# Kernel optimization log

Hardware: AMD Instinct MI355X
Metric: run time of the kernel (lower is better)

## Reference

```python
import jax, jax.numpy as jnp
import numpy as np

E, F, H = 8, 5632, 2048
T = 8192


def setup_inputs() -> dict:
    key = jax.random.key(0)
    k1, k2, k3, k4 = jax.random.split(key, 4)
    s_w = 1.0 / np.sqrt(H)
    return {
        "expert_idx": 3,
        "hidden_states": jax.random.normal(k1, (T, H), dtype=jnp.float32),
        "fc1_1": jax.random.normal(k2, (E, F, H), dtype=jnp.float32) * s_w,
        "fc1_2": jax.random.normal(k3, (E, F, H), dtype=jnp.float32) * s_w,
        "fc2": jax.random.normal(k4, (E, H, F), dtype=jnp.float32) * (1.0 / np.sqrt(F)),
    }


def reference(expert_idx, hidden_states, fc1_1, fc1_2, fc2):
    # Select this expert's weights: [F,H], [F,H], [H,F]
    w1 = fc1_1[expert_idx]
    w2 = fc1_2[expert_idx]
    w3 = fc2[expert_idx]
    # SwiGLU FFN: silu(x @ w1^T) * (x @ w2^T) @ w3^T
    gate = jnp.einsum("th,fh->tf", hidden_states, w1)
    up = jnp.einsum("th,fh->tf", hidden_states, w2)
    fc1_out = jax.nn.silu(gate) * up  # [T, F]
    out = jnp.einsum("tf,hf->th", fc1_out, w3)  # [T, H]
    return out
```

## Files before the change

kernel.cpp:

```cpp
#include <hip/hip_runtime.h>
#include <hip/hip_bf16.h>

#define T_DIM 8192
#define H_DIM 2048
#define F_DIM 5632

typedef __attribute__((ext_vector_type(4))) float f32x4;
typedef __attribute__((ext_vector_type(8))) short bf16x8;

static __device__ __forceinline__ void gload16(const void* g, void* l) {
    __builtin_amdgcn_global_load_lds(
        (const __attribute__((address_space(1))) void*)g,
        (__attribute__((address_space(3))) void*)l,
        16, 0, 0);
}

static __device__ __forceinline__ unsigned short f2bf(float f) {
    unsigned int u = __float_as_uint(f);
    u += 0x7fffu + ((u >> 16) & 1u);
    return (unsigned short)(u >> 16);
}

__global__ __launch_bounds__(256)
void cvt_f32_bf16(const float* __restrict__ base, const int* __restrict__ eidx,
                  long per_expert, unsigned short* __restrict__ dst, long n)
{
    const float* src = base;
    if (eidx) src += (long)(*eidx) * per_expert;
    const long stride = (long)gridDim.x * blockDim.x;
    for (long i = (long)blockIdx.x * blockDim.x + threadIdx.x; i * 4 < n; i += stride) {
        const float4 v = *(const float4*)(src + i * 4);
        ushort4 o;
        o.x = f2bf(v.x); o.y = f2bf(v.y); o.z = f2bf(v.z); o.w = f2bf(v.w);
        *(ushort4*)(dst + i * 4) = o;
    }
}

static __device__ __forceinline__ void stage_half(const unsigned short* __restrict__ g,
                                                  long grow0, long ldk, long kb,
                                                  unsigned short* l, int t, int i0)
{
    const int r  = t >> 3;
    const int cc = ((t & 7) ^ (r & 7)) << 3;
    #pragma unroll
    for (int i = i0; i < i0 + 2; ++i)
        gload16(g + (grow0 + i * 64 + r) * ldk + kb + cc,
                l + i * 4096 + t * 8);
}

static __device__ __forceinline__ bf16x8 ldsfrag(const unsigned short* base,
                                                 int row, int kk, int q)
{
    return *(const bf16x8*)(base + row * 64 + (((kk * 4 + q) ^ (row & 7)) << 3));
}

#define PHASE_BODY(p, STAGE_STMT)                                              \
    {                                                                          \
        bf16x8 af[2][2];                                                       \
        _Pragma("unroll")                                                      \
        for (int l_ = 0; l_ < 2; ++l_)                                         \
            _Pragma("unroll")                                                  \
            for (int kk = 0; kk < 2; ++kk)                                     \
                af[l_][kk] = ldsfrag(la, wm * 128 + (p) * 32 + l_ * 16 + lr, kk, q); \
        STAGE_STMT;                                                            \
        __builtin_amdgcn_s_barrier();                                          \
        __builtin_amdgcn_s_setprio(1);                                         \
        _Pragma("unroll")                                                      \
        for (int l_ = 0; l_ < 2; ++l_)                                         \
            _Pragma("unroll")                                                  \
            for (int ni = 0; ni < 4; ++ni)                                     \
                _Pragma("unroll")                                              \
                for (int kk = 0; kk < 2; ++kk)                                 \
                    acc[(p) * 2 + l_][ni] = __builtin_amdgcn_mfma_f32_16x16x32_bf16( \
                        af[l_][kk], bf[ni][kk], acc[(p) * 2 + l_][ni], 0, 0, 0);     \
        __builtin_amdgcn_s_setprio(0);                                         \
        __builtin_amdgcn_s_barrier();                                          \
    }

__global__ __launch_bounds__(512, 2)
void gemm1_swiglu(const unsigned short* __restrict__ X,
                  const unsigned short* __restrict__ W1,
                  const unsigned short* __restrict__ W2,
                  unsigned short* __restrict__ Hout)
{
    __shared__ __align__(16) unsigned short sAll[4 * 16384];

    const int tid  = threadIdx.x;
    const int lane = tid & 63;
    const int wid  = tid >> 6;
    const int wm   = wid >> 2;
    const int wn   = wid & 3;
    const int q    = lane >> 4;
    const int lr   = lane & 15;

    const int nwg = gridDim.x;
    const int bid = blockIdx.x;
    const int cpx = nwg >> 3;
    const int swz = (bid & 7) * cpx + (bid >> 3);
    const int NBN = F_DIM / 128;
    const int bm  = swz / NBN;
    const int bn  = swz % NBN;

    const long arow0 = (long)bm * 256;
    const long b1r0  = (long)bn * 128;
    const long b2r0  = (long)bn * 128 - 128;
    const int  NK    = H_DIM / 64;

    f32x4 acc[8][4] = {};

    stage_half(X,  arow0, H_DIM, 0, sAll,          tid, 0);
    stage_half(X,  arow0, H_DIM, 0, sAll,          tid, 2);
    stage_half(W1, b1r0,  H_DIM, 0, sAll + 16384,  tid, 0);
    stage_half(W2, b2r0,  H_DIM, 0, sAll + 16384,  tid, 2);
    stage_half(W1, b1r0,  H_DIM, 64, sAll + 49152, tid, 0);
    stage_half(W2, b2r0,  H_DIM, 64, sAll + 49152, tid, 2);

    for (int j = 0; j < NK; ++j) {
        unsigned short* la = sAll + (j & 1) * 32768;
        unsigned short* lb = la + 16384;

        if (j + 1 < NK) {
            unsigned short* na = sAll + ((j + 1) & 1) * 32768;
            stage_half(X, arow0, H_DIM, (long)(j + 1) * 64, na, tid, 0);
            stage_half(X, arow0, H_DIM, (long)(j + 1) * 64, na, tid, 2);
            asm volatile("s_waitcnt vmcnt(8)" ::: "memory");
        } else {
            asm volatile("s_waitcnt vmcnt(0)" ::: "memory");
        }
        __builtin_amdgcn_s_barrier();

        bf16x8 bf[4][2];
        #pragma unroll
        for (int ni = 0; ni < 4; ++ni)
            #pragma unroll
            for (int kk = 0; kk < 2; ++kk)
                bf[ni][kk] = ldsfrag(lb, wn * 64 + ni * 16 + lr, kk, q);

        PHASE_BODY(0, {})
        PHASE_BODY(1, { if (j + 2 < NK) stage_half(W1, b1r0, H_DIM, (long)(j + 2) * 64, lb, tid, 0); })
        PHASE_BODY(2, { if (j + 2 < NK) stage_half(W2, b2r0, H_DIM, (long)(j + 2) * 64, lb, tid, 2); })
        PHASE_BODY(3, {})
    }

    float* slab = (float*)sAll;
    float* s = slab + (wm * 2 + (wn & 1)) * 8192;
    if (wn >= 2) {
        #pragma unroll
        for (int mi = 0; mi < 8; ++mi)
            #pragma unroll
            for (int ni = 0; ni < 4; ++ni)
                #pragma unroll
                for (int r = 0; r < 4; ++r)
                    s[(mi * 16 + q * 4 + r) * 64 + ni * 16 + lr] = acc[mi][ni][r];
    }
    __syncthreads();
    if (wn < 2) {
        const long orow = (long)bm * 256 + wm * 128;
        const long ocol = (long)bn * 128 + wn * 64;
        #pragma unroll
        for (int mi = 0; mi < 8; ++mi)
            #pragma unroll
            for (int ni = 0; ni < 4; ++ni)
                #pragma unroll
                for (int r = 0; r < 4; ++r) {
                    const float g = acc[mi][ni][r];
                    const float u = s[(mi * 16 + q * 4 + r) * 64 + ni * 16 + lr];
                    const float h = (g / (1.0f + __expf(-g))) * u;
                    Hout[(orow + mi * 16 + q * 4 + r) * F_DIM + (ocol + ni * 16 + lr)] = f2bf(h);
                }
    }
}

__global__ __launch_bounds__(512, 2)
void gemm2_out(const unsigned short* __restrict__ A,
               const unsigned short* __restrict__ B,
               float* __restrict__ Out)
{
    __shared__ __align__(16) unsigned short sAll[4 * 16384];

    const int tid  = threadIdx.x;
    const int lane = tid & 63;
    const int wid  = tid >> 6;
    const int wm   = wid >> 2;
    const int wn   = wid & 3;
    const int q    = lane >> 4;
    const int lr   = lane & 15;

    const int nwg = gridDim.x;
    const int bid = blockIdx.x;
    const int cpx = nwg >> 3;
    const int swz = (bid & 7) * cpx + (bid >> 3);
    const int NBN = H_DIM / 256;
    const int bm  = swz / NBN;
    const int bn  = swz % NBN;

    const long arow0 = (long)bm * 256;
    const long brow0 = (long)bn * 256;
    const int  NK    = F_DIM / 64;

    f32x4 acc[8][4] = {};

    stage_half(A, arow0, F_DIM, 0, sAll,          tid, 0);
    stage_half(A, arow0, F_DIM, 0, sAll,          tid, 2);
    stage_half(B, brow0, F_DIM, 0, sAll + 16384,  tid, 0);
    stage_half(B, brow0, F_DIM, 0, sAll + 16384,  tid, 2);
    stage_half(B, brow0, F_DIM, 64, sAll + 49152, tid, 0);
    stage_half(B, brow0, F_DIM, 64, sAll + 49152, tid, 2);

    for (int j = 0; j < NK; ++j) {
        unsigned short* la = sAll + (j & 1) * 32768;
        unsigned short* lb = la + 16384;

        if (j + 1 < NK) {
            unsigned short* na = sAll + ((j + 1) & 1) * 32768;
            stage_half(A, arow0, F_DIM, (long)(j + 1) * 64, na, tid, 0);
            stage_half(A, arow0, F_DIM, (long)(j + 1) * 64, na, tid, 2);
            asm volatile("s_waitcnt vmcnt(8)" ::: "memory");
        } else {
            asm volatile("s_waitcnt vmcnt(0)" ::: "memory");
        }
        __builtin_amdgcn_s_barrier();

        bf16x8 bf[4][2];
        #pragma unroll
        for (int ni = 0; ni < 4; ++ni)
            #pragma unroll
            for (int kk = 0; kk < 2; ++kk)
                bf[ni][kk] = ldsfrag(lb, wn * 64 + ni * 16 + lr, kk, q);

        PHASE_BODY(0, {})
        PHASE_BODY(1, { if (j + 2 < NK) stage_half(B, brow0, F_DIM, (long)(j + 2) * 64, lb, tid, 0); })
        PHASE_BODY(2, { if (j + 2 < NK) stage_half(B, brow0, F_DIM, (long)(j + 2) * 64, lb, tid, 2); })
        PHASE_BODY(3, {})
    }

    const long orow = (long)bm * 256 + wm * 128;
    const long ocol = (long)bn * 256 + wn * 64;
    #pragma unroll
    for (int mi = 0; mi < 8; ++mi)
        #pragma unroll
        for (int ni = 0; ni < 4; ++ni)
            #pragma unroll
            for (int r = 0; r < 4; ++r)
                Out[(orow + mi * 16 + q * 4 + r) * H_DIM + (ocol + ni * 16 + lr)] = acc[mi][ni][r];
}

extern "C" void kernel_launch(void* const* d_in, const int* in_sizes, int n_in,
                              void* d_out, int out_size, void* d_ws, size_t ws_size,
                              hipStream_t stream)
{
    const int*   eidx = (const int*)d_in[0];
    const float* x    = (const float*)d_in[1];
    const float* w1   = (const float*)d_in[2];
    const float* w2   = (const float*)d_in[3];
    const float* w3   = (const float*)d_in[4];
    float* out = (float*)d_out;

    unsigned short* Xb  = (unsigned short*)d_ws;
    unsigned short* W1b = Xb  + (long)T_DIM * H_DIM;
    unsigned short* W2b = W1b + (long)F_DIM * H_DIM;
    unsigned short* W3b = W2b + (long)F_DIM * H_DIM;
    unsigned short* Hb  = W3b + (long)H_DIM * F_DIM;

    cvt_f32_bf16<<<2048, 256, 0, stream>>>(x,  nullptr, 0, Xb, (long)T_DIM * H_DIM);
    cvt_f32_bf16<<<2048, 256, 0, stream>>>(w1, eidx, (long)F_DIM * H_DIM, W1b, (long)F_DIM * H_DIM);
    cvt_f32_bf16<<<2048, 256, 0, stream>>>(w2, eidx, (long)F_DIM * H_DIM, W2b, (long)F_DIM * H_DIM);
    cvt_f32_bf16<<<2048, 256, 0, stream>>>(w3, eidx, (long)H_DIM * F_DIM, W3b, (long)H_DIM * F_DIM);

    gemm1_swiglu<<<(T_DIM / 256) * (F_DIM / 128), 512, 0, stream>>>(Xb, W1b, W2b, Hb);
    gemm2_out  <<<(T_DIM / 256) * (H_DIM / 256), 512, 0, stream>>>(Hb, W3b, out);
}
```

Measured before the change: 588.9 us.

## Split fused gate/up GEMM into two separate GEMMs with bf16 gate round-trip

Replaces the fused gate+up GEMM, which packed 128 columns of W1 and 128 of W2 into one 256-wide tile, with a templated 256x256 GEMM launched twice. The first launch writes the gate result to the H buffer as bf16. The second computes the up projection, reads the gate back, applies SiLU and writes H in place. This drops the LDS exchange and the epilogue where half the waves sat idle, but X is now read twice and the intermediate makes an extra bf16 global round-trip. The gate is also rounded to bf16 before SiLU, which adds a small precision loss.

```diff
diff --git a/kernel.cpp b/kernel.cpp
--- a/kernel.cpp
+++ b/kernel.cpp
@@ -19,6 +19,10 @@
     unsigned int u = __float_as_uint(f);
     u += 0x7fffu + ((u >> 16) & 1u);
     return (unsigned short)(u >> 16);
+}
+
+static __device__ __forceinline__ float bf2f(unsigned short u) {
+    return __uint_as_float(((unsigned int)u) << 16);
 }
 
 __global__ __launch_bounds__(256)
@@ -77,12 +81,15 @@
         __builtin_amdgcn_s_barrier();                                          \
     }
 
+template<int MODE, int KDIM, int NBN>
 __global__ __launch_bounds__(512, 2)
-void gemm1_swiglu(const unsigned short* __restrict__ X,
-                  const unsigned short* __restrict__ W1,
-                  const unsigned short* __restrict__ W2,
-                  unsigned short* __restrict__ Hout)
+void gemm256(const unsigned short* __restrict__ A,
+             const unsigned short* __restrict__ B,
+             void* outp, const unsigned short* gate)
 {
+    constexpr int  NK   = KDIM / 64;
+    constexpr long NTOT = (long)NBN * 256;
+
     __shared__ __align__(16) unsigned short sAll[4 * 16384];
 
     const int tid  = threadIdx.x;
@@ -97,23 +104,20 @@
     const int bid = blockIdx.x;
     const int cpx = nwg >> 3;
     const int swz = (bid & 7) * cpx + (bid >> 3);
-    const int NBN = F_DIM / 128;
     const int bm  = swz / NBN;
     const int bn  = swz % NBN;
 
     const long arow0 = (long)bm * 256;
-    const long b1r0  = (long)bn * 128;
-    const long b2r0  = (long)bn * 128 - 128;
-    const int  NK    = H_DIM / 64;
+    const long brow0 = (long)bn * 256;
 
     f32x4 acc[8][4] = {};
 
-    stage_half(X,  arow0, H_DIM, 0, sAll,          tid, 0);
-    stage_half(X,  arow0, H_DIM, 0, sAll,          tid, 2);
-    stage_half(W1, b1r0,  H_DIM, 0, sAll + 16384,  tid, 0);
-    stage_half(W2, b2r0,  H_DIM, 0, sAll + 16384,  tid, 2);
-    stage_half(W1, b1r0,  H_DIM, 64, sAll + 49152, tid, 0);
-    stage_half(W2, b2r0,  H_DIM, 64, sAll + 49152, tid, 2);
+    stage_half(A, arow0, KDIM, 0,  sAll,          tid, 0);
+    stage_half(A, arow0, KDIM, 0,  sAll,          tid, 2);
+    stage_half(B, brow0, KDIM, 0,  sAll + 16384,  tid, 0);
+    stage_half(B, brow0, KDIM, 0,  sAll + 16384,  tid, 2);
+    stage_half(B, brow0, KDIM, 64, sAll + 49152,  tid, 0);
+    stage_half(B, brow0, KDIM, 64, sAll + 49152,  tid, 2);
 
     for (int j = 0; j < NK; ++j) {
         unsigned short* la = sAll + (j & 1) * 32768;
@@ -121,8 +125,8 @@
 
         if (j + 1 < NK) {
             unsigned short* na = sAll + ((j + 1) & 1) * 32768;
-            stage_half(X, arow0, H_DIM, (long)(j + 1) * 64, na, tid, 0);
-            stage_half(X, arow0, H_DIM, (long)(j + 1) * 64, na, tid, 2);
+            stage_half(A, arow0, KDIM, (long)(j + 1) * 64, na, tid, 0);
+            stage_half(A, arow0, KDIM, (long)(j + 1) * 64, na, tid, 2);
             asm volatile("s_waitcnt vmcnt(8)" ::: "memory");
         } else {
             asm volatile("s_waitcnt vmcnt(0)" ::: "memory");
@@ -137,100 +141,8 @@
                 bf[ni][kk] = ldsfrag(lb, wn * 64 + ni * 16 + lr, kk, q);
 
         PHASE_BODY(0, {})
-        PHASE_BODY(1, { if (j + 2 < NK) stage_half(W1, b1r0, H_DIM, (long)(j + 2) * 64, lb, tid, 0); })
-        PHASE_BODY(2, { if (j + 2 < NK) stage_half(W2, b2r0, H_DIM, (long)(j + 2) * 64, lb, tid, 2); })
-        PHASE_BODY(3, {})
-    }
-
-    float* slab = (float*)sAll;
-    float* s = slab + (wm * 2 + (wn & 1)) * 8192;
-    if (wn >= 2) {
-        #pragma unroll
-        for (int mi = 0; mi < 8; ++mi)
-            #pragma unroll
-            for (int ni = 0; ni < 4; ++ni)
-                #pragma unroll
-                for (int r = 0; r < 4; ++r)
-                    s[(mi * 16 + q * 4 + r) * 64 + ni * 16 + lr] = acc[mi][ni][r];
-    }
-    __syncthreads();
-    if (wn < 2) {
-        const long orow = (long)bm * 256 + wm * 128;
-        const long ocol = (long)bn * 128 + wn * 64;
-        #pragma unroll
-        for (int mi = 0; mi < 8; ++mi)
-            #pragma unroll
-            for (int ni = 0; ni < 4; ++ni)
-                #pragma unroll
-                for (int r = 0; r < 4; ++r) {
-                    const float g = acc[mi][ni][r];
-                    const float u = s[(mi * 16 + q * 4 + r) * 64 + ni * 16 + lr];
-                    const float h = (g / (1.0f + __expf(-g))) * u;
-                    Hout[(orow + mi * 16 + q * 4 + r) * F_DIM + (ocol + ni * 16 + lr)] = f2bf(h);
-                }
-    }
-}
-
-__global__ __launch_bounds__(512, 2)
-void gemm2_out(const unsigned short* __restrict__ A,
-               const unsigned short* __restrict__ B,
-               float* __restrict__ Out)
-{
-    __shared__ __align__(16) unsigned short sAll[4 * 16384];
-
-    const int tid  = threadIdx.x;
-    const int lane = tid & 63;
-    const int wid  = tid >> 6;
-    const int wm   = wid >> 2;
-    const int wn   = wid & 3;
-    const int q    = lane >> 4;
-    const int lr   = lane & 15;
-
-    const int nwg = gridDim.x;
-    const int bid = blockIdx.x;
-    const int cpx = nwg >> 3;
-    const int swz = (bid & 7) * cpx + (bid >> 3);
-    const int NBN = H_DIM / 256;
-    const int bm  = swz / NBN;
-    const int bn  = swz % NBN;
-
-    const long arow0 = (long)bm * 256;
-    const long brow0 = (long)bn * 256;
-    const int  NK    = F_DIM / 64;
-
-    f32x4 acc[8][4] = {};
-
-    stage_half(A, arow0, F_DIM, 0, sAll,          tid, 0);
-    stage_half(A, arow0, F_DIM, 0, sAll,          tid, 2);
-    stage_half(B, brow0, F_DIM, 0, sAll + 16384,  tid, 0);
-    stage_half(B, brow0, F_DIM, 0, sAll + 16384,  tid, 2);
-    stage_half(B, brow0, F_DIM, 64, sAll + 49152, tid, 0);
-    stage_half(B, brow0, F_DIM, 64, sAll + 49152, tid, 2);
-
-    for (int j = 0; j < NK; ++j) {
-        unsigned short* la = sAll + (j & 1) * 32768;
-        unsigned short* lb = la + 16384;
-
-        if (j + 1 < NK) {
-            unsigned short* na = sAll + ((j + 1) & 1) * 32768;
-            stage_half(A, arow0, F_DIM, (long)(j + 1) * 64, na, tid, 0);
-            stage_half(A, arow0, F_DIM, (long)(j + 1) * 64, na, tid, 2);
-            asm volatile("s_waitcnt vmcnt(8)" ::: "memory");
-        } else {
-            asm volatile("s_waitcnt vmcnt(0)" ::: "memory");
-        }
-        __builtin_amdgcn_s_barrier();
-
-        bf16x8 bf[4][2];
-        #pragma unroll
-        for (int ni = 0; ni < 4; ++ni)
-            #pragma unroll
-            for (int kk = 0; kk < 2; ++kk)
-                bf[ni][kk] = ldsfrag(lb, wn * 64 + ni * 16 + lr, kk, q);
-
-        PHASE_BODY(0, {})
-        PHASE_BODY(1, { if (j + 2 < NK) stage_half(B, brow0, F_DIM, (long)(j + 2) * 64, lb, tid, 0); })
-        PHASE_BODY(2, { if (j + 2 < NK) stage_half(B, brow0, F_DIM, (long)(j + 2) * 64, lb, tid, 2); })
+        PHASE_BODY(1, { if (j + 2 < NK) stage_half(B, brow0, KDIM, (long)(j + 2) * 64, lb, tid, 0); })
+        PHASE_BODY(2, { if (j + 2 < NK) stage_half(B, brow0, KDIM, (long)(j + 2) * 64, lb, tid, 2); })
         PHASE_BODY(3, {})
     }
 
@@ -241,8 +153,18 @@
         #pragma unroll
         for (int ni = 0; ni < 4; ++ni)
             #pragma unroll
-            for (int r = 0; r < 4; ++r)
-                Out[(orow + mi * 16 + q * 4 + r) * H_DIM + (ocol + ni * 16 + lr)] = acc[mi][ni][r];
+            for (int r = 0; r < 4; ++r) {
+                const long idx = (orow + mi * 16 + q * 4 + r) * NTOT + (ocol + ni * 16 + lr);
+                if constexpr (MODE == 0) {
+                    ((float*)outp)[idx] = acc[mi][ni][r];
+                } else if constexpr (MODE == 1) {
+                    ((unsigned short*)outp)[idx] = f2bf(acc[mi][ni][r]);
+                } else {
+                    const float g = bf2f(gate[idx]);
+                    const float h = __fdividef(g, 1.0f + __expf(-g)) * acc[mi][ni][r];
+                    ((unsigned short*)outp)[idx] = f2bf(h);
+                }
+            }
 }
 
 extern "C" void kernel_launch(void* const* d_in, const int* in_sizes, int n_in,
@@ -267,6 +189,10 @@
     cvt_f32_bf16<<<2048, 256, 0, stream>>>(w2, eidx, (long)F_DIM * H_DIM, W2b, (long)F_DIM * H_DIM);
     cvt_f32_bf16<<<2048, 256, 0, stream>>>(w3, eidx, (long)H_DIM * F_DIM, W3b, (long)H_DIM * F_DIM);
 
-    gemm1_swiglu<<<(T_DIM / 256) * (F_DIM / 128), 512, 0, stream>>>(Xb, W1b, W2b, Hb);
-    gemm2_out  <<<(T_DIM / 256) * (H_DIM / 256), 512, 0, stream>>>(Hb, W3b, out);
+    gemm256<1, H_DIM, F_DIM / 256><<<(T_DIM / 256) * (F_DIM / 256), 512, 0, stream>>>(
+        Xb, W1b, Hb, nullptr);
+    gemm256<2, H_DIM, F_DIM / 256><<<(T_DIM / 256) * (F_DIM / 256), 512, 0, stream>>>(
+        Xb, W2b, Hb, Hb);
+    gemm256<0, F_DIM, H_DIM / 256><<<(T_DIM / 256) * (H_DIM / 256), 512, 0, stream>>>(
+        Hb, W3b, out, nullptr);
 }
```

Measured after the change: 637.1 us. 1.08x slower.
